# Performance work log

Measured on AMD Instinct MI355X. Metric: run time of the kernel, lower is better.

The kernel has to match this reference:

```python
import jax, jax.numpy as jnp
import numpy as np

EMB_DIM = 1024
SEQ = 2048
BATCH = 4


def setup_inputs() -> dict:
    key = jax.random.key(0)
    k1, k2, k3, k4, k5 = jax.random.split(key, 5)
    Q = jax.random.normal(k1, (SEQ, BATCH, EMB_DIM), dtype=jnp.float32)
    K = jax.random.normal(k2, (SEQ, BATCH, EMB_DIM), dtype=jnp.float32)
    V = jax.random.normal(k3, (SEQ, BATCH, EMB_DIM), dtype=jnp.float32)
    # nn.Linear default init scale ~ 1/sqrt(fan_in)
    W_in = jax.random.normal(k4, (3 * EMB_DIM, EMB_DIM), dtype=jnp.float32) / np.sqrt(EMB_DIM)
    W_out = jax.random.normal(k5, (EMB_DIM, EMB_DIM), dtype=jnp.float32) / np.sqrt(EMB_DIM)
    return {"Q": Q, "K": K, "V": V, "W_in": W_in, "W_out": W_out}


def reference(Q, K, V, W_in, W_out):
    # NOTE: original module ignores K and V args entirely (self-attention on Q).
    emb = Q.shape[-1]
    scale = 1.0 / np.sqrt(emb)
    qkv = jnp.einsum('sbe,fe->sbf', Q, W_in)        # [S, B, 3E]
    q, k, v = jnp.split(qkv, 3, axis=-1)            # each [S, B, E]
    q = jnp.transpose(q, (1, 0, 2)) * scale         # [B, S, E]
    k = jnp.transpose(k, (1, 0, 2))                 # [B, S, E]
    v = jnp.transpose(v, (1, 0, 2))                 # [B, S, E]
    scores = jnp.einsum('bte,bse->bts', q, k)       # [B, T, S]
    # per-target-row softmax over source dim == vectorized softmax on last axis
    weights = jax.nn.softmax(scores, axis=-1)       # [B, T, S]
    out = jnp.einsum('bts,bse->bte', weights, v)    # [B, T, E]
    out = jnp.transpose(out, (1, 0, 2))             # [T, B, E]
    out = jnp.einsum('tbe,fe->tbf', out, W_out)     # [T, B, E]
    return (out, weights)
```

## Files before the change

### kernel.cpp

```cpp
#include <hip/hip_runtime.h>
#include <stdint.h>

typedef unsigned short u16;
typedef __bf16 bf16_t;
typedef bf16_t bf16x8 __attribute__((ext_vector_type(8)));
typedef float f32x4 __attribute__((ext_vector_type(4)));
typedef u16 u16x4 __attribute__((ext_vector_type(4)));
typedef u16 u16x8 __attribute__((ext_vector_type(8)));

#define AS1 __attribute__((address_space(1)))
#define AS3 __attribute__((address_space(3)))

__device__ __forceinline__ u16 f2bf(float f) {
  union { float f; uint32_t u; } x; x.f = f;
  uint32_t u = x.u;
  return (u16)((u + 0x7fffu + ((u >> 16) & 1u)) >> 16);
}

__device__ __forceinline__ float bf2f(u16 b) {
  union { uint32_t u; float f; } x; x.u = ((uint32_t)b) << 16;
  return x.f;
}

__device__ __forceinline__ void gload_lds16(const void* g, void* lds) {
  __builtin_amdgcn_global_load_lds((const AS1 uint32_t*)g, (AS3 uint32_t*)lds, 16, 0, 0);
}

__device__ __forceinline__ void xcd_remap(int& bx, int& by, int& bz) {
  const int gx = gridDim.x, gy = gridDim.y;
  const int n = gx * gy * gridDim.z;
  const int lin = blockIdx.x + gx * (blockIdx.y + gy * blockIdx.z);
  const int q = n >> 3;
  const int work = (lin & 7) * q + (lin >> 3);
  bx = work % gx;
  const int t = work / gx;
  by = t % gy;
  bz = t / gy;
}

__global__ __launch_bounds__(256) void cvt_bf16(const float* __restrict__ in,
                                                u16* __restrict__ out, int n4) {
  int i = blockIdx.x * 256 + threadIdx.x;
  if (i >= n4) return;
  float4 v = ((const float4*)in)[i];
  u16x4 o = {f2bf(v.x), f2bf(v.y), f2bf(v.z), f2bf(v.w)};
  *(u16x4*)(out + (size_t)i * 4) = o;
}

#define BARRIER() do { asm volatile("" ::: "memory"); \
                       __builtin_amdgcn_s_barrier();  \
                       asm volatile("" ::: "memory"); } while (0)

#define MQS(MQi, NQi, ASET, BSET)                                              \
  do {                                                                         \
    __builtin_amdgcn_s_setprio(1);                                             \
    _Pragma("unroll") for (int j_ = 0; j_ < 4; ++j_) {                         \
      _Pragma("unroll") for (int i_ = 0; i_ < 2; ++i_) {                       \
        acc[(MQi) * 4 + j_][(NQi) * 2 + i_] =                                  \
            __builtin_amdgcn_mfma_f32_16x16x32_bf16(                           \
                ASET[j_][0], BSET[i_][0],                                      \
                acc[(MQi) * 4 + j_][(NQi) * 2 + i_], 0, 0, 0);                 \
        acc[(MQi) * 4 + j_][(NQi) * 2 + i_] =                                  \
            __builtin_amdgcn_mfma_f32_16x16x32_bf16(                           \
                ASET[j_][1], BSET[i_][1],                                      \
                acc[(MQi) * 4 + j_][(NQi) * 2 + i_], 0, 0, 0);                 \
      }                                                                        \
    }                                                                          \
    __builtin_amdgcn_s_setprio(0);                                             \
  } while (0)

template <bool BF16OUT>
__global__ __launch_bounds__(512, 2)
void gemm256(const u16* __restrict__ A, const u16* __restrict__ B,
             void* __restrict__ Cv,
             int lda, int ldb, int ldc,
             long long sAz, long long sBz, long long sCz,
             int K, float alpha) {
  __shared__ u16 As[2][256 * 64];
  __shared__ u16 Bs[2][256 * 64];
  int bx, by, bz;
  xcd_remap(bx, by, bz);
  const int tid  = threadIdx.x;
  const int lane = tid & 63;
  const int wid  = tid >> 6;
  const int wr   = wid >> 2;
  const int wc   = wid & 3;
  const long long z = bz;
  const u16* Ab = A + z * sAz;
  const u16* Bb = B + z * sBz;
  const int rowBase = by * 256;
  const int colBase = bx * 256;
  const int nt = K >> 6;

  const int sRow   = tid >> 3;
  const int sChunk = (tid & 7) ^ (sRow & 7);
  const size_t ldaS = (size_t)lda, ldbS = (size_t)ldb;
  const u16* aS = Ab + (size_t)(rowBase + sRow) * ldaS + sChunk * 8;
  const u16* bS = Bb + (size_t)(colBase + sRow) * ldbS + sChunk * 8;

  const int fr = lane & 15;
  const int kx = lane >> 4;
  const int rx = lane & 7;

  f32x4 acc[8][4];
  const f32x4 zf = {0.f, 0.f, 0.f, 0.f};
#pragma unroll
  for (int m = 0; m < 8; ++m)
#pragma unroll
    for (int n = 0; n < 4; ++n) acc[m][n] = zf;

  bf16x8 Ara[4][2], Arb[4][2], Bra[2][2], Brb[2][2];

  auto stageA = [&](int buf, int h, int kt) {
    const u16* s = aS + (size_t)(h * 128) * ldaS + kt;
    char* d = ((char*)&As[buf][0]) + h * 16384 + tid * 16;
    gload_lds16(s, d);
    gload_lds16(s + 64 * ldaS, d + 8192);
  };
  auto stageB = [&](int buf, int h, int kt) {
    const u16* s = bS + (size_t)(h * 128) * ldbS + kt;
    char* d = ((char*)&Bs[buf][0]) + h * 16384 + tid * 16;
    gload_lds16(s, d);
    gload_lds16(s + 64 * ldbS, d + 8192);
  };
  auto ldsA = [&](int buf, int mq, bf16x8 (&dst)[4][2]) {
#pragma unroll
    for (int j = 0; j < 4; ++j) {
      const int row = mq * 128 + wr * 64 + j * 16 + fr;
#pragma unroll
      for (int k = 0; k < 2; ++k) {
        const int ch = ((k * 4 + kx) ^ rx) * 8;
        dst[j][k] = *(const bf16x8*)&As[buf][row * 64 + ch];
      }
    }
  };
  auto ldsB = [&](int buf, int nq, bf16x8 (&dst)[2][2]) {
#pragma unroll
    for (int i = 0; i < 2; ++i) {
      const int row = nq * 128 + i * 64 + wc * 16 + fr;
#pragma unroll
      for (int k = 0; k < 2; ++k) {
        const int ch = ((k * 4 + kx) ^ rx) * 8;
        dst[i][k] = *(const bf16x8*)&Bs[buf][row * 64 + ch];
      }
    }
  };

  stageA(0, 0, 0);
  stageA(0, 1, 0);
  stageB(0, 0, 0);
  stageB(0, 1, 0);
  asm volatile("s_waitcnt vmcnt(0)" ::: "memory");
  BARRIER();
  ldsA(0, 0, Ara);
  ldsB(0, 0, Bra);

  for (int t = 0; t < nt; ++t) {
    const int c = t & 1;
    const int kt1 = (t + 1) << 6;
    const bool s1 = (t + 1 < nt);
    ldsB(c, 1, Brb);
    ldsA(c, 1, Arb);
    if (s1) {
      stageA(1 - c, 0, kt1);
      stageA(1 - c, 1, kt1);
      stageB(1 - c, 0, kt1);
      stageB(1 - c, 1, kt1);
    }
    MQS(0, 0, Ara, Bra);
    MQS(0, 1, Ara, Brb);
    if (s1) {
      asm volatile("s_waitcnt lgkmcnt(0)" ::: "memory");
      asm volatile("s_waitcnt vmcnt(0)" ::: "memory");
      BARRIER();
      ldsA(1 - c, 0, Ara);
      __builtin_amdgcn_sched_barrier(0);
    }
    MQS(1, 0, Arb, Bra);
    if (s1) ldsB(1 - c, 0, Bra);
    MQS(1, 1, Arb, Brb);
  }

  const int r0 = (lane >> 4) * 4;
#pragma unroll
  for (int m = 0; m < 8; ++m) {
    const int grow = rowBase + (m >> 2) * 128 + wr * 64 + (m & 3) * 16 + r0;
#pragma unroll
    for (int jj = 0; jj < 4; ++jj) {
      const size_t rOff = (size_t)(grow + jj) * (size_t)ldc;
      if constexpr (BF16OUT) {
        u16* C = (u16*)Cv + z * sCz;
#pragma unroll
        for (int n = 0; n < 4; ++n) {
          const int gcol = colBase + (n >> 1) * 128 + (n & 1) * 64 + wc * 16 + fr;
          C[rOff + gcol] = f2bf(acc[m][n][jj] * alpha);
        }
      } else {
        float* C = (float*)Cv + z * sCz;
#pragma unroll
        for (int n = 0; n < 4; ++n) {
          const int gcol = colBase + (n >> 1) * 128 + (n & 1) * 64 + wc * 16 + fr;
          C[rOff + gcol] = acc[m][n][jj] * alpha;
        }
      }
    }
  }
}

template <bool BF16OUT>
__global__ __launch_bounds__(512, 2)
void gemm128(const u16* __restrict__ A, const u16* __restrict__ B,
             void* __restrict__ Cv,
             int lda, int ldb, int ldc,
             long long sAz, long long sBz, long long sCz,
             int K, float alpha) {
  __shared__ u16 As[2][128 * 64];
  __shared__ u16 Bs[2][256 * 64];
  int bx, by, bz;
  xcd_remap(bx, by, bz);
  const int tid  = threadIdx.x;
  const int lane = tid & 63;
  const int wid  = tid >> 6;
  const int wr   = wid >> 2;
  const int wc   = wid & 3;
  const long long z = bz;
  const u16* Ab = A + z * sAz;
  const u16* Bb = B + z * sBz;
  const int rowBase = by * 128;
  const int colBase = bx * 256;
  const int nt = K >> 6;

  const int sRow   = tid >> 3;
  const int sChunk = (tid & 7) ^ (sRow & 7);
  const size_t ldaS = (size_t)lda, ldbS = (size_t)ldb;
  const u16* aS = Ab + (size_t)(rowBase + sRow) * ldaS + sChunk * 8;
  const u16* bS = Bb + (size_t)(colBase + sRow) * ldbS + sChunk * 8;

  const int fr = lane & 15;
  const int kx = lane >> 4;
  const int rx = lane & 7;

  f32x4 acc[4][4];
  const f32x4 zf = {0.f, 0.f, 0.f, 0.f};
#pragma unroll
  for (int m = 0; m < 4; ++m)
#pragma unroll
    for (int n = 0; n < 4; ++n) acc[m][n] = zf;

  bf16x8 Ara[4][2], Arb[4][2], Bra[2][2], Brb[2][2];

  auto stageA = [&](int buf, int kt) {
    const u16* s = aS + kt;
    char* d = ((char*)&As[buf][0]) + tid * 16;
    gload_lds16(s, d);
    gload_lds16(s + 64 * ldaS, d + 8192);
  };
  auto stageB = [&](int buf, int h, int kt) {
    const u16* s = bS + (size_t)(h * 128) * ldbS + kt;
    char* d = ((char*)&Bs[buf][0]) + h * 16384 + tid * 16;
    gload_lds16(s, d);
    gload_lds16(s + 64 * ldbS, d + 8192);
  };
  auto ldsA = [&](int buf, bf16x8 (&dst)[4][2]) {
#pragma unroll
    for (int j = 0; j < 4; ++j) {
      const int row = wr * 64 + j * 16 + fr;
#pragma unroll
      for (int k = 0; k < 2; ++k) {
        const int ch = ((k * 4 + kx) ^ rx) * 8;
        dst[j][k] = *(const bf16x8*)&As[buf][row * 64 + ch];
      }
    }
  };
  auto ldsB = [&](int buf, int nq, bf16x8 (&dst)[2][2]) {
#pragma unroll
    for (int i = 0; i < 2; ++i) {
      const int row = nq * 128 + i * 64 + wc * 16 + fr;
#pragma unroll
      for (int k = 0; k < 2; ++k) {
        const int ch = ((k * 4 + kx) ^ rx) * 8;
        dst[i][k] = *(const bf16x8*)&Bs[buf][row * 64 + ch];
      }
    }
  };

  auto tile = [&](int t, int c, bf16x8 (&ACUR)[4][2], bf16x8 (&ANXT)[4][2]) {
    const int kt1 = (t + 1) << 6;
    const bool s1 = (t + 1 < nt);
    ldsB(c, 1, Brb);
    if (s1) {
      stageA(1 - c, kt1);
      stageB(1 - c, 0, kt1);
      stageB(1 - c, 1, kt1);
    }
    MQS(0, 0, ACUR, Bra);
    if (s1) {
      asm volatile("s_waitcnt lgkmcnt(0)" ::: "memory");
      asm volatile("s_waitcnt vmcnt(0)" ::: "memory");
      BARRIER();
      ldsA(1 - c, ANXT);
      ldsB(1 - c, 0, Bra);
      __builtin_amdgcn_sched_barrier(0);
    }
    MQS(0, 1, ACUR, Brb);
  };

  stageA(0, 0);
  stageB(0, 0, 0);
  stageB(0, 1, 0);
  asm volatile("s_waitcnt vmcnt(0)" ::: "memory");
  BARRIER();
  ldsA(0, Ara);
  ldsB(0, 0, Bra);

  for (int tt = 0; tt < nt; tt += 2) {
    tile(tt,     0, Ara, Arb);
    tile(tt + 1, 1, Arb, Ara);
  }

  const int r0 = (lane >> 4) * 4;
#pragma unroll
  for (int m = 0; m < 4; ++m) {
    const int grow = rowBase + wr * 64 + m * 16 + r0;
#pragma unroll
    for (int jj = 0; jj < 4; ++jj) {
      const size_t rOff = (size_t)(grow + jj) * (size_t)ldc;
      if constexpr (BF16OUT) {
        u16* C = (u16*)Cv + z * sCz;
#pragma unroll
        for (int n = 0; n < 4; ++n) {
          const int gcol = colBase + (n >> 1) * 128 + (n & 1) * 64 + wc * 16 + fr;
          C[rOff + gcol] = f2bf(acc[m][n][jj] * alpha);
        }
      } else {
        float* C = (float*)Cv + z * sCz;
#pragma unroll
        for (int n = 0; n < 4; ++n) {
          const int gcol = colBase + (n >> 1) * 128 + (n & 1) * 64 + wc * 16 + fr;
          C[rOff + gcol] = acc[m][n][jj] * alpha;
        }
      }
    }
  }
}

__global__ __launch_bounds__(256)
void softmax_rows(u16* __restrict__ sbf, float* __restrict__ wfp) {
  const size_t row = blockIdx.x;
  const int tid = threadIdx.x;
  u16* pb = sbf + row * 2048;
  u16x8 xb = *(const u16x8*)(pb + tid * 8);
  float x[8];
#pragma unroll
  for (int j = 0; j < 8; ++j) x[j] = bf2f(xb[j]);
  float m = x[0];
#pragma unroll
  for (int j = 1; j < 8; ++j) m = fmaxf(m, x[j]);
#pragma unroll
  for (int o = 32; o; o >>= 1) m = fmaxf(m, __shfl_xor(m, o, 64));
  __shared__ float red[8];
  if ((tid & 63) == 0) red[tid >> 6] = m;
  __syncthreads();
  m = fmaxf(fmaxf(red[0], red[1]), fmaxf(red[2], red[3]));
  float e[8];
  float s = 0.f;
#pragma unroll
  for (int j = 0; j < 8; ++j) { e[j] = expf(x[j] - m); s += e[j]; }
#pragma unroll
  for (int o = 32; o; o >>= 1) s += __shfl_xor(s, o, 64);
  if ((tid & 63) == 0) red[4 + (tid >> 6)] = s;
  __syncthreads();
  s = (red[4] + red[5]) + (red[6] + red[7]);
  const float inv = 1.0f / s;
  float w[8];
#pragma unroll
  for (int j = 0; j < 8; ++j) w[j] = e[j] * inv;
  float* pf = wfp + row * 2048;
  float4 o0 = {w[0], w[1], w[2], w[3]};
  float4 o1 = {w[4], w[5], w[6], w[7]};
  ((float4*)pf)[tid * 2] = o0;
  ((float4*)pf)[tid * 2 + 1] = o1;
  u16x8 ub;
#pragma unroll
  for (int j = 0; j < 8; ++j) ub[j] = f2bf(w[j]);
  *(u16x8*)(pb + tid * 8) = ub;
}

extern "C" void kernel_launch(void* const* d_in, const int* in_sizes, int n_in,
                              void* d_out, int out_size, void* d_ws, size_t ws_size,
                              hipStream_t stream) {
  const float* Q  = (const float*)d_in[0];
  const float* Wi = (const float*)d_in[3];
  const float* Wo = (const float*)d_in[4];
  float* out0    = (float*)d_out;
  float* weights = out0 + (size_t)2048 * 4 * 1024;

  char* ws = (char*)d_ws;
  u16* Qb   = (u16*)(ws);
  u16* Wib  = (u16*)(ws + ((size_t)16 << 20));
  u16* Wob  = (u16*)(ws + ((size_t)22 << 20));
  u16* qkvb = (u16*)(ws + ((size_t)24 << 20));
  u16* vwT  = (u16*)(ws + ((size_t)72 << 20));
  u16* wbf  = (u16*)(ws + ((size_t)88 << 20));

  cvt_bf16<<<dim3(8192), dim3(256), 0, stream>>>(Q,  Qb,  2097152);
  cvt_bf16<<<dim3(3072), dim3(256), 0, stream>>>(Wi, Wib, 786432);
  cvt_bf16<<<dim3(1024), dim3(256), 0, stream>>>(Wo, Wob, 262144);

  gemm256<true><<<dim3(8, 32, 1), dim3(512), 0, stream>>>(
      Qb, Wib, (void*)qkvb, 1024, 1024, 3072, 0, 0, 0, 1024, 1.0f);

  gemm128<true><<<dim3(4, 64, 1), dim3(512), 0, stream>>>(
      Qb, Wib + (size_t)2048 * 1024, (void*)(qkvb + 2048),
      1024, 1024, 3072, 0, 0, 0, 1024, 1.0f);

  gemm256<true><<<dim3(8, 8, 4), dim3(512), 0, stream>>>(
      qkvb, qkvb + 1024, (void*)wbf, 12288, 12288, 2048,
      3072LL, 3072LL, 4194304LL, 1024, 0.03125f);

  gemm128<true><<<dim3(8, 8, 4), dim3(512), 0, stream>>>(
      Wob, qkvb + 2048, (void*)vwT, 1024, 12288, 2048,
      0LL, 3072LL, 2097152LL, 1024, 1.0f);

  softmax_rows<<<dim3(8192), dim3(256), 0, stream>>>(wbf, weights);

  gemm128<false><<<dim3(4, 16, 4), dim3(512), 0, stream>>>(
      wbf, vwT, (void*)out0, 2048, 2048, 4096,
      4194304LL, 2097152LL, 1024LL, 2048, 1.0f);
}
```

Measured before the change: 197.4 us.

## Split-K final P·V GEMM with 256-tile kernel and atomic accumulation

Replaces the final weights×(V·Wo^T) gemm128 launch with a new 256x256-tile kernel that splits K=2048 into two halves across the z grid dimension, accumulating into the fp32 output with atomicAdd. The output is zeroed by a memset first. The aim is a larger tile with more data reuse while keeping enough blocks (4x8x8 = 256) to fill the GPU. The cost is an extra memset pass, float atomic traffic, and a summation order that is no longer deterministic.

Measured after the change: 243.5 us. +23.4%, slower.

```diff
diff --git a/kernel.cpp b/kernel.cpp
--- a/kernel.cpp
+++ b/kernel.cpp
@@ -207,6 +207,135 @@
   }
 }
 
+__global__ __launch_bounds__(512, 2)
+void gemm256_ksplit(const u16* __restrict__ A, const u16* __restrict__ B,
+                    float* __restrict__ Cf,
+                    int lda, int ldb, int ldc,
+                    long long sAz, long long sBz, long long sCz,
+                    int Khalf, float alpha) {
+  __shared__ u16 As[2][256 * 64];
+  __shared__ u16 Bs[2][256 * 64];
+  int bx, by, bz;
+  xcd_remap(bx, by, bz);
+  const int tid  = threadIdx.x;
+  const int lane = tid & 63;
+  const int wid  = tid >> 6;
+  const int wr   = wid >> 2;
+  const int wc   = wid & 3;
+  const long long b  = bz >> 1;
+  const int kh = bz & 1;
+  const u16* Ab = A + b * sAz + (size_t)kh * Khalf;
+  const u16* Bb = B + b * sBz + (size_t)kh * Khalf;
+  const int rowBase = by * 256;
+  const int colBase = bx * 256;
+  const int nt = Khalf >> 6;
+
+  const int sRow   = tid >> 3;
+  const int sChunk = (tid & 7) ^ (sRow & 7);
+  const size_t ldaS = (size_t)lda, ldbS = (size_t)ldb;
+  const u16* aS = Ab + (size_t)(rowBase + sRow) * ldaS + sChunk * 8;
+  const u16* bS = Bb + (size_t)(colBase + sRow) * ldbS + sChunk * 8;
+
+  const int fr = lane & 15;
+  const int kx = lane >> 4;
+  const int rx = lane & 7;
+
+  f32x4 acc[8][4];
+  const f32x4 zf = {0.f, 0.f, 0.f, 0.f};
+#pragma unroll
+  for (int m = 0; m < 8; ++m)
+#pragma unroll
+    for (int n = 0; n < 4; ++n) acc[m][n] = zf;
+
+  bf16x8 Ara[4][2], Arb[4][2], Bra[2][2], Brb[2][2];
+
+  auto stageA = [&](int buf, int h, int kt) {
+    const u16* s = aS + (size_t)(h * 128) * ldaS + kt;
+    char* d = ((char*)&As[buf][0]) + h * 16384 + tid * 16;
+    gload_lds16(s, d);
+    gload_lds16(s + 64 * ldaS, d + 8192);
+  };
+  auto stageB = [&](int buf, int h, int kt) {
+    const u16* s = bS + (size_t)(h * 128) * ldbS + kt;
+    char* d = ((char*)&Bs[buf][0]) + h * 16384 + tid * 16;
+    gload_lds16(s, d);
+    gload_lds16(s + 64 * ldbS, d + 8192);
+  };
+  auto ldsA = [&](int buf, int mq, bf16x8 (&dst)[4][2]) {
+#pragma unroll
+    for (int j = 0; j < 4; ++j) {
+      const int row = mq * 128 + wr * 64 + j * 16 + fr;
+#pragma unroll
+      for (int k = 0; k < 2; ++k) {
+        const int ch = ((k * 4 + kx) ^ rx) * 8;
+        dst[j][k] = *(const bf16x8*)&As[buf][row * 64 + ch];
+      }
+    }
+  };
+  auto ldsB = [&](int buf, int nq, bf16x8 (&dst)[2][2]) {
+#pragma unroll
+    for (int i = 0; i < 2; ++i) {
+      const int row = nq * 128 + i * 64 + wc * 16 + fr;
+#pragma unroll
+      for (int k = 0; k < 2; ++k) {
+        const int ch = ((k * 4 + kx) ^ rx) * 8;
+        dst[i][k] = *(const bf16x8*)&Bs[buf][row * 64 + ch];
+      }
+    }
+  };
+
+  stageA(0, 0, 0);
+  stageA(0, 1, 0);
+  stageB(0, 0, 0);
+  stageB(0, 1, 0);
+  asm volatile("s_waitcnt vmcnt(0)" ::: "memory");
+  BARRIER();
+  ldsA(0, 0, Ara);
+  ldsB(0, 0, Bra);
+
+  for (int t = 0; t < nt; ++t) {
+    const int c = t & 1;
+    const int kt1 = (t + 1) << 6;
+    const bool s1 = (t + 1 < nt);
+    ldsB(c, 1, Brb);
+    ldsA(c, 1, Arb);
+    if (s1) {
+      stageA(1 - c, 0, kt1);
+      stageA(1 - c, 1, kt1);
+      stageB(1 - c, 0, kt1);
+      stageB(1 - c, 1, kt1);
+    }
+    MQS(0, 0, Ara, Bra);
+    MQS(0, 1, Ara, Brb);
+    if (s1) {
+      asm volatile("s_waitcnt lgkmcnt(0)" ::: "memory");
+      asm volatile("s_waitcnt vmcnt(0)" ::: "memory");
+      BARRIER();
+      ldsA(1 - c, 0, Ara);
+      __builtin_amdgcn_sched_barrier(0);
+    }
+    MQS(1, 0, Arb, Bra);
+    if (s1) ldsB(1 - c, 0, Bra);
+    MQS(1, 1, Arb, Brb);
+  }
+
+  float* C = Cf + b * sCz;
+  const int r0 = (lane >> 4) * 4;
+#pragma unroll
+  for (int m = 0; m < 8; ++m) {
+    const int grow = rowBase + (m >> 2) * 128 + wr * 64 + (m & 3) * 16 + r0;
+#pragma unroll
+    for (int jj = 0; jj < 4; ++jj) {
+      const size_t rOff = (size_t)(grow + jj) * (size_t)ldc;
+#pragma unroll
+      for (int n = 0; n < 4; ++n) {
+        const int gcol = colBase + (n >> 1) * 128 + (n & 1) * 64 + wc * 16 + fr;
+        atomicAdd(&C[rOff + gcol], acc[m][n][jj] * alpha);
+      }
+    }
+  }
+}
+
 template <bool BF16OUT>
 __global__ __launch_bounds__(512, 2)
 void gemm128(const u16* __restrict__ A, const u16* __restrict__ B,
@@ -403,6 +532,8 @@
   u16* vwT  = (u16*)(ws + ((size_t)72 << 20));
   u16* wbf  = (u16*)(ws + ((size_t)88 << 20));
 
+  hipMemsetAsync(out0, 0, (size_t)2048 * 4 * 1024 * sizeof(float), stream);
+
   cvt_bf16<<<dim3(8192), dim3(256), 0, stream>>>(Q,  Qb,  2097152);
   cvt_bf16<<<dim3(3072), dim3(256), 0, stream>>>(Wi, Wib, 786432);
   cvt_bf16<<<dim3(1024), dim3(256), 0, stream>>>(Wo, Wob, 262144);
@@ -424,7 +555,7 @@
 
   softmax_rows<<<dim3(8192), dim3(256), 0, stream>>>(wbf, weights);
 
-  gemm128<false><<<dim3(4, 16, 4), dim3(512), 0, stream>>>(
-      wbf, vwT, (void*)out0, 2048, 2048, 4096,
-      4194304LL, 2097152LL, 1024LL, 2048, 1.0f);
-}
+  gemm256_ksplit<<<dim3(4, 8, 8), dim3(512), 0, stream>>>(
+      wbf, vwT, out0, 2048, 2048, 4096,
+      4194304LL, 2097152LL, 1024LL, 1024, 1.0f);
+}
```
